# Kernel optimization log

Hardware: AMD Instinct MI355X
Metric: run time of the kernel (lower is better)

## Reference

```python
import jax, jax.numpy as jnp
import numpy as np

NEG_INF = jnp.float32(-1e9)


def setup_inputs() -> dict:
    key = jax.random.key(0)
    k1, k2, k3 = jax.random.split(key, 3)
    B, S, L, T = 64, 1024, 16, 32
    transitions = jax.random.normal(k1, (B, S, L, T), dtype=jnp.float32)
    # tags index the flattened (seg_offset*T + tag) score view; keep seg_offset=0
    # so indices are valid for every window length (matches original gather semantics).
    tags = jax.random.randint(k2, (B, S), 0, T)
    lens = jax.random.randint(k3, (B,), 1, S + 1)  # lens in [1, S]
    return {"transitions": transitions, "tags": tags, "lens": lens}


def _semi_crf_loss(transitions, tags, lens):
    # transitions: [B, S, L, T]; tags: [B, S]; lens: [B]
    B, S, L, T = transitions.shape
    # alpha padded with L-1 leading -inf entries so the length-L reversed window
    # alpha[e-L:e] (with out-of-range entries excluded) is a fixed-size slice.
    # pad index p corresponds to alpha index p-(L-1); alpha[0] = 0.
    pad0 = jnp.full((B, S + L), NEG_INF, dtype=transitions.dtype).at[:, L - 1].set(0.0)

    trans_tm = jnp.moveaxis(transitions, 1, 0)  # [S, B, L, T] time-major
    tags_tm = tags.T.astype(jnp.int32)          # [S, B]

    def step(carry, xs):
        a_num, a_den = carry                      # [B, S+L] each
        e_idx, tr, tg = xs                        # tr: [B, L, T], tg: [B]
        # reversed window: alpha_rev[k] = alpha[e-1-k], e = e_idx + 1
        w_den = jax.lax.dynamic_slice(a_den, (0, e_idx), (B, L))[:, ::-1]
        w_num = jax.lax.dynamic_slice(a_num, (0, e_idx), (B, L))[:, ::-1]
        f_den = (w_den[:, :, None] + tr).reshape(B, L * T)  # [B, L*T]
        f_num = (w_num[:, :, None] + tr).reshape(B, L * T)
        den_new = jax.nn.logsumexp(f_den, axis=1)
        num_new = jnp.take_along_axis(f_num, tg[:, None], axis=1)[:, 0]
        a_den = jax.lax.dynamic_update_slice(a_den, den_new[:, None], (0, e_idx + L))
        a_num = jax.lax.dynamic_update_slice(a_num, num_new[:, None], (0, e_idx + L))
        return (a_num, a_den), None

    (a_num, a_den), _ = jax.lax.scan(step, (pad0, pad0), (jnp.arange(S), trans_tm, tags_tm))

    idx = (lens + (L - 1)).astype(jnp.int32)[:, None]   # alpha[lens] in padded coords
    numerator = jnp.take_along_axis(a_num, idx, axis=1)[:, 0]
    denominator = jnp.take_along_axis(a_den, idx, axis=1)[:, 0]
    return jnp.sum(denominator - numerator)


def reference(transitions, tags, lens):
    return _semi_crf_loss(transitions, tags, lens)
```

## Files before the change

kernel.cpp:

```cpp
#include <hip/hip_runtime.h>

#define B_ 64
#define S_ 1024
#define L_ 16
#define T_ 32
#define CH 32
#define NC (S_ / CH)

__device__ __forceinline__ float fexp2(float x) { return __builtin_amdgcn_exp2f(x); }
__device__ __forceinline__ float flog2(float x) { return __builtin_amdgcn_logf(x); }

template <int CTRL, bool BC>
__device__ __forceinline__ float dpp_mov_f(float x) {
    int xi = __float_as_int(x);
    int r = __builtin_amdgcn_update_dpp(xi, xi, CTRL, 0xF, 0xF, BC);
    return __int_as_float(r);
}
__device__ __forceinline__ float dpp_shr1_fill(float x, float fill) {
    int xi = __float_as_int(x), fi = __float_as_int(fill);
    int r = __builtin_amdgcn_update_dpp(fi, xi, 0x111, 0xF, 0xF, false);
    return __int_as_float(r);
}
__device__ __forceinline__ float row16_sum(float t) {
    t += dpp_mov_f<0xB1, true>(t);
    t += dpp_mov_f<0x4E, true>(t);
    t += dpp_mov_f<0x124, true>(t);
    t += dpp_mov_f<0x128, true>(t);
    return t;
}
__device__ __forceinline__ float row16_max(float t) {
    t = fmaxf(t, dpp_mov_f<0xB1, true>(t));
    t = fmaxf(t, dpp_mov_f<0x4E, true>(t));
    t = fmaxf(t, dpp_mov_f<0x124, true>(t));
    t = fmaxf(t, dpp_mov_f<0x128, true>(t));
    return t;
}

__global__ __launch_bounds__(256) void p1_kernel(const float* __restrict__ tr,
                                                 const int* __restrict__ tags,
                                                 const int* __restrict__ lens,
                                                 float* __restrict__ Mg,
                                                 float* __restrict__ R2t,
                                                 float* __restrict__ numc,
                                                 float* __restrict__ out) {
    __shared__ float R2s[CH * L_];
    const int bc = blockIdx.x;
    const int b = bc >> 5, c = bc & 31;
    const int tid = threadIdx.x;
    if (bc == 0 && tid == 0) out[0] = 0.f;

    const int len = lens[b];
    const float LOG2E = 1.4426950408889634f;

    const float4* tr4 = reinterpret_cast<const float4*>(tr);
    const size_t base4 = ((size_t)b * 16384 + (size_t)c * 512) * 8;
#pragma unroll 8
    for (int pass = 0; pass < 16; ++pass) {
        float4 v = tr4[base4 + (size_t)pass * 256 + tid];
        float s = fexp2(v.x * LOG2E) + fexp2(v.y * LOG2E) +
                  fexp2(v.z * LOG2E) + fexp2(v.w * LOG2E);
        s += dpp_mov_f<0xB1, true>(s);
        s += dpp_mov_f<0x4E, true>(s);
        s += dpp_mov_f<0x141, true>(s);
        if ((tid & 7) == 0) R2s[pass * 32 + (tid >> 3)] = flog2(s);
    }

    if (tid < 64) {
        float nm = 0.f;
        if (tid < 32) {
            int s = c * 32 + tid;
            if (s < len) {
                int tg = tags[b * S_ + s];
                nm = tr[(((size_t)b * S_ + s) * L_) * T_ + tg];
            }
        }
        for (int off = 32; off > 0; off >>= 1) nm += __shfl_xor(nm, off, 64);
        if (tid == 0) numc[b * NC + c] = nm;
    }
    __syncthreads();

    if (c == (len >> 5)) {
        R2t[b * 512 + tid] = R2s[tid];
        R2t[b * 512 + 256 + tid] = R2s[256 + tid];
    }

    const int G = tid >> 4;
    const int kk = tid & 15;
    float a2 = R2s[G];
    float wp = (kk == 0) ? 0.f : ((kk == G + 1) ? -a2 : -1e9f);
#pragma unroll 4
    for (int row = 1; row < CH; ++row) {
        float x = wp + R2s[row * 16 + kk];
        float t = fexp2(x);
        t = row16_sum(t);
        float d = flog2(t);
        a2 += d;
        wp = dpp_shr1_fill(wp, d) - d;
    }
    Mg[(size_t)bc * 256 + kk * 16 + G] = a2 + wp;
}

__global__ __launch_bounds__(256) void p2_kernel(const float* __restrict__ Mg,
                                                 const float* __restrict__ R2t,
                                                 const float* __restrict__ numc,
                                                 const int* __restrict__ lens,
                                                 float* __restrict__ out) {
    __shared__ float Ms[NC * 256];
    __shared__ float R2l[CH * L_];
    __shared__ float vb[2][16];
    __shared__ float numsh;
    const int b = blockIdx.x, tid = threadIdx.x;
    const int len = lens[b];
    const int q = len >> 5, r = len & 31;

    {
        const float4* Mg4 = reinterpret_cast<const float4*>(Mg + (size_t)b * NC * 256);
        float4* Ms4 = reinterpret_cast<float4*>(Ms);
#pragma unroll
        for (int i = 0; i < 8; ++i) Ms4[i * 256 + tid] = Mg4[i * 256 + tid];
    }
    R2l[tid] = R2t[b * 512 + tid];
    R2l[256 + tid] = R2t[b * 512 + 256 + tid];
    if (tid < 64) {
        float nm = (tid < 32) ? numc[b * NC + tid] : 0.f;
        for (int off = 32; off > 0; off >>= 1) nm += __shfl_xor(nm, off, 64);
        if (tid == 0) numsh = nm;
    }
    if (tid < 16) vb[0][tid] = (tid == 0) ? 0.f : -1e9f;
    __syncthreads();

    int p = 0;
    const int i16 = tid >> 4, j = tid & 15;
    for (int c = 0; c < q; ++c) {
        float vj = vb[p][j], v0 = vb[p][0];
        float x = Ms[c * 256 + tid] + vj - v0;
        float mx = row16_max(x);
        float t = row16_sum(fexp2(x - mx));
        float nv = v0 + mx + flog2(t);
        if (j == 0) vb[1 - p][i16] = nv;
        __syncthreads();
        p ^= 1;
    }

    if (tid < 64) {
        const int kk = tid & 15;
        float v0 = vb[p][0];
        float wp = vb[p][kk] - v0;
        float a2 = v0;
        for (int t0 = 0; t0 < r; ++t0) {
            float x = wp + R2l[t0 * 16 + kk];
            float e = fexp2(x);
            e = row16_sum(e);
            float d = flog2(e);
            a2 += d;
            wp = dpp_shr1_fill(wp, d) - d;
        }
        if (tid == 0) atomicAdd(out, a2 * 0.6931471805599453f - numsh);
    }
}

extern "C" void kernel_launch(void* const* d_in, const int* in_sizes, int n_in,
                              void* d_out, int out_size, void* d_ws, size_t ws_size,
                              hipStream_t stream) {
    const float* tr = (const float*)d_in[0];
    const int* tags = (const int*)d_in[1];
    const int* lens = (const int*)d_in[2];
    float* out = (float*)d_out;

    float* Mg = (float*)d_ws;
    float* R2t = Mg + (size_t)B_ * NC * 256;
    float* numc = R2t + (size_t)B_ * 512;

    p1_kernel<<<B_ * NC, 256, 0, stream>>>(tr, tags, lens, Mg, R2t, numc, out);
    p2_kernel<<<B_, 256, 0, stream>>>(Mg, R2t, numc, lens, out);
}
```

Baseline: 205.8 us.

## Fuse second pass into first kernel via per-batch last-block ticket

Removes the separate p2 kernel launch. Each chunk block increments a per-batch atomic counter, and the last block to finish for a batch runs the cross-chunk combine and the tail recurrence, reading Mg and R2t directly from global memory instead of staging them in LDS. Two memsets are added to reset the counter and the output. This trades a kernel launch and a global barrier for threadfences, atomics, extra memset launches, and uncached serial global reads in the combine loop.

```diff
diff --git a/kernel.cpp b/kernel.cpp
--- a/kernel.cpp
+++ b/kernel.cpp
@@ -42,13 +42,15 @@
                                                  float* __restrict__ Mg,
                                                  float* __restrict__ R2t,
                                                  float* __restrict__ numc,
+                                                 int* __restrict__ cnt,
                                                  float* __restrict__ out) {
     __shared__ float R2s[CH * L_];
+    __shared__ float vb[2][16];
+    __shared__ float numsh;
+    __shared__ int ticket_s;
     const int bc = blockIdx.x;
     const int b = bc >> 5, c = bc & 31;
     const int tid = threadIdx.x;
-    if (bc == 0 && tid == 0) out[0] = 0.f;
-
     const int len = lens[b];
     const float LOG2E = 1.4426950408889634f;
 
@@ -86,41 +88,29 @@
 
     const int G = tid >> 4;
     const int kk = tid & 15;
-    float a2 = R2s[G];
-    float wp = (kk == 0) ? 0.f : ((kk == G + 1) ? -a2 : -1e9f);
+    {
+        float a2 = R2s[G];
+        float wp = (kk == 0) ? 0.f : ((kk == G + 1) ? -a2 : -1e9f);
 #pragma unroll 4
-    for (int row = 1; row < CH; ++row) {
-        float x = wp + R2s[row * 16 + kk];
-        float t = fexp2(x);
-        t = row16_sum(t);
-        float d = flog2(t);
-        a2 += d;
-        wp = dpp_shr1_fill(wp, d) - d;
+        for (int row = 1; row < CH; ++row) {
+            float x = wp + R2s[row * 16 + kk];
+            float t = fexp2(x);
+            t = row16_sum(t);
+            float d = flog2(t);
+            a2 += d;
+            wp = dpp_shr1_fill(wp, d) - d;
+        }
+        Mg[(size_t)bc * 256 + kk * 16 + G] = a2 + wp;
     }
-    Mg[(size_t)bc * 256 + kk * 16 + G] = a2 + wp;
-}
 
-__global__ __launch_bounds__(256) void p2_kernel(const float* __restrict__ Mg,
-                                                 const float* __restrict__ R2t,
-                                                 const float* __restrict__ numc,
-                                                 const int* __restrict__ lens,
-                                                 float* __restrict__ out) {
-    __shared__ float Ms[NC * 256];
-    __shared__ float R2l[CH * L_];
-    __shared__ float vb[2][16];
-    __shared__ float numsh;
-    const int b = blockIdx.x, tid = threadIdx.x;
-    const int len = lens[b];
+    __threadfence();
+    __syncthreads();
+    if (tid == 0) ticket_s = atomicAdd(&cnt[b], 1);
+    __syncthreads();
+    if (ticket_s != NC - 1) return;
+    __threadfence();
+
     const int q = len >> 5, r = len & 31;
-
-    {
-        const float4* Mg4 = reinterpret_cast<const float4*>(Mg + (size_t)b * NC * 256);
-        float4* Ms4 = reinterpret_cast<float4*>(Ms);
-#pragma unroll
-        for (int i = 0; i < 8; ++i) Ms4[i * 256 + tid] = Mg4[i * 256 + tid];
-    }
-    R2l[tid] = R2t[b * 512 + tid];
-    R2l[256 + tid] = R2t[b * 512 + 256 + tid];
     if (tid < 64) {
         float nm = (tid < 32) ? numc[b * NC + tid] : 0.f;
         for (int off = 32; off > 0; off >>= 1) nm += __shfl_xor(nm, off, 64);
@@ -131,9 +121,10 @@
 
     int p = 0;
     const int i16 = tid >> 4, j = tid & 15;
-    for (int c = 0; c < q; ++c) {
+    const float* Mb = Mg + (size_t)b * NC * 256;
+    for (int cc = 0; cc < q; ++cc) {
         float vj = vb[p][j], v0 = vb[p][0];
-        float x = Ms[c * 256 + tid] + vj - v0;
+        float x = Mb[cc * 256 + tid] + vj - v0;
         float mx = row16_max(x);
         float t = row16_sum(fexp2(x - mx));
         float nv = v0 + mx + flog2(t);
@@ -143,13 +134,12 @@
     }
 
     if (tid < 64) {
-        const int kk = tid & 15;
         float v0 = vb[p][0];
         float wp = vb[p][kk] - v0;
         float a2 = v0;
+        const float* Rl = R2t + b * 512;
         for (int t0 = 0; t0 < r; ++t0) {
-            float x = wp + R2l[t0 * 16 + kk];
-            float e = fexp2(x);
+            float e = fexp2(wp + Rl[t0 * 16 + kk]);
             e = row16_sum(e);
             float d = flog2(e);
             a2 += d;
@@ -170,7 +160,9 @@
     float* Mg = (float*)d_ws;
     float* R2t = Mg + (size_t)B_ * NC * 256;
     float* numc = R2t + (size_t)B_ * 512;
+    int* cnt = (int*)(numc + (size_t)B_ * NC);
 
-    p1_kernel<<<B_ * NC, 256, 0, stream>>>(tr, tags, lens, Mg, R2t, numc, out);
-    p2_kernel<<<B_, 256, 0, stream>>>(Mg, R2t, numc, lens, out);
+    hipMemsetAsync(cnt, 0, B_ * sizeof(int), stream);
+    hipMemsetAsync(out, 0, sizeof(float), stream);
+    p1_kernel<<<B_ * NC, 256, 0, stream>>>(tr, tags, lens, Mg, R2t, numc, cnt, out);
 }
```

Result: slower. 431.2 us (+109.6%).
